# Optimization experiments

Hardware: AMD Instinct MI355X
Metric: run time of the kernel (lower is better)

The kernel has to match this reference:

```python
import jax, jax.numpy as jnp
import numpy as np

B, S, H = 32, 4096, 1024
EPS = 1e-12

def setup_inputs() -> dict:
    key = jax.random.key(0)
    k1, k2, k3, k4 = jax.random.split(key, 4)
    x = jax.random.normal(k1, (B, S, H), dtype=jnp.float32)
    # mask: random bool; force the first two positions True per row so every
    # row has >=2 masked elements (std with ddof=1 is well-defined)
    mask = jax.random.randint(k2, (B, S), 0, 2).astype(bool)
    mask = mask.at[:, :2].set(True)
    W = jax.random.normal(k3, (H,), dtype=jnp.float32) / np.sqrt(H)
    b = jax.random.normal(k4, (1,), dtype=jnp.float32) * 0.01
    return {"input": x, "mask": mask, "W": W, "b": b}

def reference(input, mask, W, b):
    # linear projection hidden_size -> 1, then squeeze -> [B, S]
    h = jnp.einsum("bsh,h->bs", input, W) + b  # [B, S]
    mf = mask.astype(h.dtype)
    n = mf.sum(axis=-1, keepdims=True)                      # [B, 1]
    mean = (h * mf).sum(axis=-1, keepdims=True) / n         # masked mean
    # torch .std() on the masked slice: unbiased (ddof=1)
    var = (((h - mean) ** 2) * mf).sum(axis=-1, keepdims=True) / (n - 1)
    std = jnp.sqrt(var) + EPS
    z = (h - mean) / std
    zmin = jnp.min(jnp.where(mask, z, jnp.inf), axis=-1, keepdims=True)
    zmax = jnp.max(jnp.where(mask, z, -jnp.inf), axis=-1, keepdims=True)
    rescaled = (z - zmin) / (zmax - zmin)
    return (rescaled * mf)[..., None]  # [B, S, 1]
```

## Files before the change

### kernel.cpp

```cpp
#include <hip/hip_runtime.h>

#define BB 32
#define SS 4096
#define HH 1024
#define BS (BB * SS)
#define WPB 256
#define RPW (SS / WPB)
#define NWAVES (BB * WPB)
#define NBLOCKS (NWAVES / 4)

__device__ __forceinline__ unsigned fkey(float f) {
    unsigned u = __float_as_uint(f);
    return (u & 0x80000000u) ? ~u : (u | 0x80000000u);
}
__device__ __forceinline__ float funkey(unsigned k) {
    unsigned u = (k & 0x80000000u) ? (k ^ 0x80000000u) : ~k;
    return __uint_as_float(u);
}
__device__ __forceinline__ float dot4(float4 a, float4 w) {
    return a.x * w.x + a.y * w.y + a.z * w.z + a.w * w.w;
}

__global__ __launch_bounds__(256) void k_proj(
    const float* __restrict__ x, const int* __restrict__ mask,
    const float* __restrict__ W, const float* __restrict__ bvec,
    float* __restrict__ h, unsigned* __restrict__ mm)
{
    const int lane  = threadIdx.x & 63;
    const int gw    = blockIdx.x * 4 + (threadIdx.x >> 6);
    const int batch = gw >> 8;
    const int r0    = gw & (WPB - 1);

    const float4* Wv = (const float4*)W;
    const float4 w0 = Wv[lane], w1 = Wv[64 + lane],
                 w2 = Wv[128 + lane], w3 = Wv[192 + lane];
    const float bval = bvec[0];

    const size_t rowBase = (size_t)batch * SS;
    unsigned kmin = 0xFFFFFFFFu, kmax = 0u;

    const float4* xr = (const float4*)(x + (rowBase + r0) * HH);
    float4 a0 = xr[lane], a1 = xr[64 + lane], a2 = xr[128 + lane], a3 = xr[192 + lane];

    for (int k = 0; k < RPW; ++k) {
        const int r = r0 + k * WPB;
        float4 b0, b1, b2, b3;
        if (k < RPW - 1) {
            const float4* xn = (const float4*)(x + (rowBase + r + WPB) * HH);
            b0 = xn[lane]; b1 = xn[64 + lane]; b2 = xn[128 + lane]; b3 = xn[192 + lane];
        }
        float acc = dot4(a0, w0) + dot4(a1, w1) + dot4(a2, w2) + dot4(a3, w3);
#pragma unroll
        for (int off = 32; off >= 1; off >>= 1)
            acc += __shfl_xor(acc, off, 64);
        const float hv = acc + bval;
        if (lane == 0) h[rowBase + r] = hv;
        if (mask[rowBase + r] != 0) {
            const unsigned key = fkey(hv);
            kmin = min(kmin, key); kmax = max(kmax, key);
        }
        a0 = b0; a1 = b1; a2 = b2; a3 = b3;
    }
    if (lane == 0) {
        atomicMin(&mm[batch], kmin);
        atomicMax(&mm[BB + batch], kmax);
    }
}

__global__ __launch_bounds__(256) void k_final(
    const float* __restrict__ h, const int* __restrict__ mask,
    const unsigned* __restrict__ mm, float* __restrict__ out)
{
    const int i = blockIdx.x * 256 + threadIdx.x;
    if (i >= BS) return;
    const int batch = i >> 12;
    const float hmin = funkey(mm[batch]);
    const float hmax = funkey(mm[BB + batch]);
    const float inv = 1.0f / (hmax - hmin);
    const float v = (h[i] - hmin) * inv;
    out[i] = (mask[i] != 0) ? v : 0.0f;
}

extern "C" void kernel_launch(void* const* d_in, const int* in_sizes, int n_in,
                              void* d_out, int out_size, void* d_ws, size_t ws_size,
                              hipStream_t stream) {
    const float* x    = (const float*)d_in[0];
    const int*   mask = (const int*)d_in[1];
    const float* W    = (const float*)d_in[2];
    const float* bv   = (const float*)d_in[3];
    float* out = (float*)d_out;

    float*    h  = (float*)d_ws;
    unsigned* mm = (unsigned*)((char*)d_ws + (size_t)BS * 4);

    hipMemsetAsync(mm, 0xFF, BB * sizeof(unsigned), stream);
    hipMemsetAsync(mm + BB, 0x00, BB * sizeof(unsigned), stream);

    k_proj<<<NBLOCKS, 256, 0, stream>>>(x, mask, W, bv, h, mm);
    k_final<<<(BS + 255) / 256, 256, 0, stream>>>(h, mask, mm, out);
}
```

Before: 714.1 us.

## Batch 16 contiguous rows per wave with all loads issued upfront, vectorize finalize

Each wave now handles 16 contiguous rows instead of 16 strided ones. It issues all row loads for a chunk of the hidden dimension before accumulating, which raises memory-level parallelism compared with the one-row-ahead prefetch. Min and max are combined across the wave by shuffles, max is tracked as a min over negated keys, and a single memset initialises both. The finalize kernel uses float4/int4 vector accesses. The cost is higher register pressure from 16 float4 loads in flight, which may reduce occupancy.

New measurement: 715.9 us. About the same (+0.3%).

```diff
diff --git a/kernel.cpp b/kernel.cpp
--- a/kernel.cpp
+++ b/kernel.cpp
@@ -4,10 +4,9 @@
 #define SS 4096
 #define HH 1024
 #define BS (BB * SS)
-#define WPB 256
-#define RPW (SS / WPB)
-#define NWAVES (BB * WPB)
-#define NBLOCKS (NWAVES / 4)
+#define RPW 16
+#define WPB (SS / RPW)
+#define NBLOCKS (BB * WPB / 4)
 
 __device__ __forceinline__ unsigned fkey(float f) {
     unsigned u = __float_as_uint(f);
@@ -29,56 +28,78 @@
     const int lane  = threadIdx.x & 63;
     const int gw    = blockIdx.x * 4 + (threadIdx.x >> 6);
     const int batch = gw >> 8;
-    const int r0    = gw & (WPB - 1);
+    const int rowStart = (batch << 12) + (gw & 255) * RPW;
 
     const float4* Wv = (const float4*)W;
     const float4 w0 = Wv[lane], w1 = Wv[64 + lane],
                  w2 = Wv[128 + lane], w3 = Wv[192 + lane];
-    const float bval = bvec[0];
 
-    const size_t rowBase = (size_t)batch * SS;
-    unsigned kmin = 0xFFFFFFFFu, kmax = 0u;
+    float acc[RPW];
+#pragma unroll
+    for (int k = 0; k < RPW; ++k) acc[k] = 0.0f;
 
-    const float4* xr = (const float4*)(x + (rowBase + r0) * HH);
-    float4 a0 = xr[lane], a1 = xr[64 + lane], a2 = xr[128 + lane], a3 = xr[192 + lane];
+    const float4* xr = (const float4*)x + (size_t)rowStart * (HH / 4) + lane;
 
+#pragma unroll
+    for (int j = 0; j < 4; ++j) {
+        const float4 wj = (j == 0) ? w0 : (j == 1) ? w1 : (j == 2) ? w2 : w3;
+        float4 v[RPW];
+#pragma unroll
+        for (int k = 0; k < RPW; ++k)
+            v[k] = xr[k * (HH / 4) + j * 64];
+#pragma unroll
+        for (int k = 0; k < RPW; ++k)
+            acc[k] += dot4(v[k], wj);
+    }
+
+    float hsel = 0.0f;
+#pragma unroll
     for (int k = 0; k < RPW; ++k) {
-        const int r = r0 + k * WPB;
-        float4 b0, b1, b2, b3;
-        if (k < RPW - 1) {
-            const float4* xn = (const float4*)(x + (rowBase + r + WPB) * HH);
-            b0 = xn[lane]; b1 = xn[64 + lane]; b2 = xn[128 + lane]; b3 = xn[192 + lane];
-        }
-        float acc = dot4(a0, w0) + dot4(a1, w1) + dot4(a2, w2) + dot4(a3, w3);
+        float s = acc[k];
 #pragma unroll
         for (int off = 32; off >= 1; off >>= 1)
-            acc += __shfl_xor(acc, off, 64);
-        const float hv = acc + bval;
-        if (lane == 0) h[rowBase + r] = hv;
-        if (mask[rowBase + r] != 0) {
-            const unsigned key = fkey(hv);
-            kmin = min(kmin, key); kmax = max(kmax, key);
+            s += __shfl_xor(s, off, 64);
+        if (lane == k) hsel = s;
+    }
+
+    const float hv = hsel + bvec[0];
+    unsigned kmin = 0xFFFFFFFFu, kneg = 0xFFFFFFFFu;
+    if (lane < RPW) {
+        h[rowStart + lane] = hv;
+        if (mask[rowStart + lane] != 0) {
+            kmin = fkey(hv);
+            kneg = fkey(-hv);
         }
-        a0 = b0; a1 = b1; a2 = b2; a3 = b3;
+    }
+#pragma unroll
+    for (int off = 32; off >= 1; off >>= 1) {
+        kmin = min(kmin, (unsigned)__shfl_xor((int)kmin, off, 64));
+        kneg = min(kneg, (unsigned)__shfl_xor((int)kneg, off, 64));
     }
     if (lane == 0) {
         atomicMin(&mm[batch], kmin);
-        atomicMax(&mm[BB + batch], kmax);
+        atomicMin(&mm[BB + batch], kneg);
     }
 }
 
 __global__ __launch_bounds__(256) void k_final(
-    const float* __restrict__ h, const int* __restrict__ mask,
-    const unsigned* __restrict__ mm, float* __restrict__ out)
+    const float4* __restrict__ h4, const int4* __restrict__ mask4,
+    const unsigned* __restrict__ mm, float4* __restrict__ out4)
 {
     const int i = blockIdx.x * 256 + threadIdx.x;
-    if (i >= BS) return;
-    const int batch = i >> 12;
-    const float hmin = funkey(mm[batch]);
-    const float hmax = funkey(mm[BB + batch]);
-    const float inv = 1.0f / (hmax - hmin);
-    const float v = (h[i] - hmin) * inv;
-    out[i] = (mask[i] != 0) ? v : 0.0f;
+    if (i >= BS / 4) return;
+    const int batch = i >> 10;
+    const float hmin =  funkey(mm[batch]);
+    const float hmax = -funkey(mm[BB + batch]);
+    const float inv  = 1.0f / (hmax - hmin);
+    const float4 hv = h4[i];
+    const int4  mv = mask4[i];
+    float4 o;
+    o.x = mv.x ? (hv.x - hmin) * inv : 0.0f;
+    o.y = mv.y ? (hv.y - hmin) * inv : 0.0f;
+    o.z = mv.z ? (hv.z - hmin) * inv : 0.0f;
+    o.w = mv.w ? (hv.w - hmin) * inv : 0.0f;
+    out4[i] = o;
 }
 
 extern "C" void kernel_launch(void* const* d_in, const int* in_sizes, int n_in,
@@ -88,14 +109,13 @@
     const int*   mask = (const int*)d_in[1];
     const float* W    = (const float*)d_in[2];
     const float* bv   = (const float*)d_in[3];
-    float* out = (float*)d_out;
 
     float*    h  = (float*)d_ws;
     unsigned* mm = (unsigned*)((char*)d_ws + (size_t)BS * 4);
 
-    hipMemsetAsync(mm, 0xFF, BB * sizeof(unsigned), stream);
-    hipMemsetAsync(mm + BB, 0x00, BB * sizeof(unsigned), stream);
+    hipMemsetAsync(mm, 0xFF, 2 * BB * sizeof(unsigned), stream);
 
     k_proj<<<NBLOCKS, 256, 0, stream>>>(x, mask, W, bv, h, mm);
-    k_final<<<(BS + 255) / 256, 256, 0, stream>>>(h, mask, mm, out);
+    k_final<<<BS / 4 / 256, 256, 0, stream>>>((const float4*)h, (const int4*)mask,
+                                              mm, (float4*)d_out);
 }
```
